# Performance work log

Measured on AMD Instinct MI355X. Metric: run time of the kernel, lower is better.

## Reference

```python
import jax, jax.numpy as jnp
import numpy as np

B, N, F_IN, F_OUT, H, SE_DIM = 16, 1024, 64, 64, 4, 64
ALPHA = 0.2  # LeakyReLU negative slope


def setup_inputs() -> dict:
    key = jax.random.key(0)
    ks = jax.random.split(key, 8)
    x = jax.random.normal(ks[0], (B, N, F_IN), dtype=jnp.float32)
    adj = (jax.random.uniform(ks[1], (B, N, N)) < 0.05).astype(jnp.float32)
    SE = jax.random.normal(ks[2], (N, SE_DIM), dtype=jnp.float32)
    fin = F_IN + SE_DIM
    s_w = float(np.sqrt(2.0) * np.sqrt(6.0 / (fin + F_OUT)))
    s_a = float(np.sqrt(2.0) * np.sqrt(6.0 / (F_OUT + 1)))
    s_p = float(np.sqrt(2.0) * np.sqrt(6.0 / (H + H)))
    W = jax.random.uniform(ks[3], (H, fin, F_OUT), minval=-s_w, maxval=s_w, dtype=jnp.float32)
    a1 = jax.random.uniform(ks[4], (H, F_OUT), minval=-s_a, maxval=s_a, dtype=jnp.float32)
    a2 = jax.random.uniform(ks[5], (H, F_OUT), minval=-s_a, maxval=s_a, dtype=jnp.float32)
    P_l = jax.random.uniform(ks[6], (H, H), minval=-s_p, maxval=s_p, dtype=jnp.float32)
    P_w = jax.random.uniform(ks[7], (H, H), minval=-s_p, maxval=s_p, dtype=jnp.float32)
    return {"x": x, "adj": adj, "SE": SE, "W": W, "a1": a1, "a2": a2, "P_l": P_l, "P_w": P_w}


def reference(x, adj, SE, W, a1, a2, P_l, P_w):
    b, n, _ = x.shape
    # needSE: concat positional/structural embedding (repeated over batch)
    xi = jnp.concatenate([x, jnp.broadcast_to(SE[None], (b, n, SE.shape[-1]))], axis=2)
    # per-head projection: h[b,h,n,o]
    h = jnp.einsum('bnf,hfo->bhno', xi, W)
    f1 = jnp.einsum('bhno,ho->bhn', h, a1)
    f2 = jnp.einsum('bhno,ho->bhn', h, a2)
    # e[b,h,i,j] = leaky_relu(f1[i] + f2[j])
    e = jax.nn.leaky_relu(f1[:, :, :, None] + f2[:, :, None, :], negative_slope=ALPHA)
    # talking-heads mixing before softmax (P_l); softmax over the i (row/source) axis
    e = jnp.einsum('bhij,hg->bgij', e, P_l)
    att = jax.nn.softmax(e, axis=2)
    # talking-heads mixing after softmax (P_w)
    att = jnp.einsum('bgij,gh->bhij', att, P_w)
    # adjacency masking (dropout p=0 -> identity)
    att = att * adj[:, None]
    # aggregation + residual (in == out features, no downsample) + ELU
    out = jnp.einsum('bhij,bhjo->bhio', att, h)
    out = jax.nn.elu(out + x[:, None])
    bb, hh, nn_, oo = out.shape
    # concat heads along feature dim (head order preserved)
    return out.transpose(0, 2, 1, 3).reshape(bb, nn_, hh * oo)
```

## Files before the change

### kernel.cpp

```cpp
#include <hip/hip_runtime.h>
#include <hip/hip_bf16.h>

#define NB 16
#define NN 1024
#define FOUT 64
#define NH 4
#define LRELU_A 0.2f
#define CAP 192

typedef __attribute__((ext_vector_type(8))) short bf16x8;
typedef __attribute__((ext_vector_type(4))) float f32x4;

#define WFENCE() asm volatile("s_waitcnt lgkmcnt(0)" ::: "memory")

__device__ __forceinline__ float lrelu(float s) { return fmaxf(s, LRELU_A * s); }

__device__ __forceinline__ float4 min4(float4 a, float4 b) {
    return make_float4(fminf(a.x,b.x), fminf(a.y,b.y), fminf(a.z,b.z), fminf(a.w,b.w));
}
__device__ __forceinline__ float4 max4(float4 a, float4 b) {
    return make_float4(fmaxf(a.x,b.x), fmaxf(a.y,b.y), fmaxf(a.z,b.z), fmaxf(a.w,b.w));
}

__device__ __forceinline__ unsigned int pk2(float a, float b) {
    union { __hip_bfloat16 h; unsigned short u; } ua, ub;
    ua.h = __float2bfloat16(a); ub.h = __float2bfloat16(b);
    return (unsigned int)ua.u | ((unsigned int)ub.u << 16);
}
__device__ __forceinline__ unsigned short bfbits(float a) {
    union { __hip_bfloat16 h; unsigned short u; } ua;
    ua.h = __float2bfloat16(a);
    return ua.u;
}
__device__ __forceinline__ int toff(int r, int c) { return (r * 16 + (c ^ (r & 7))) * 16; }

__global__ __launch_bounds__(256) void k_prep(const float* __restrict__ W,
                                              uint4* __restrict__ WbT)
{
    int gid  = blockIdx.x * 256 + threadIdx.x;
    int col  = gid >> 4, c = gid & 15;
    int head = col >> 6, o = col & 63;
    const float* wp = W + head * 8192 + (c * 8) * 64 + o;
    float v[8];
    #pragma unroll
    for (int j = 0; j < 8; ++j) v[j] = wp[j * 64];
    uint4 outv = { pk2(v[0], v[1]), pk2(v[2], v[3]), pk2(v[4], v[5]), pk2(v[6], v[7]) };
    WbT[col * 16 + (c ^ (col & 7))] = outv;
}

__global__ __launch_bounds__(256) void k_proj(const float* __restrict__ x,
                                              const float* __restrict__ SE,
                                              const uint4* __restrict__ WbT,
                                              unsigned int* __restrict__ hbu)
{
    __shared__ char smem[49152];
    char* Ab = smem;
    char* Bb = smem + 32768;
    const int tid = threadIdx.x;
    const int rt  = blockIdx.x >> 2;
    const int ch  = blockIdx.x & 3;

    {
        const int row = tid & 127, kh = tid >> 7;
        const int rg = rt * 128 + row;
        const int bb = rg >> 10, nn = rg & 1023;
        const float4* src = (kh == 0) ? (const float4*)(x + ((size_t)(bb * NN + nn)) * 64)
                                      : (const float4*)(SE + (size_t)nn * 64);
        #pragma unroll
        for (int q = 0; q < 8; ++q) {
            float4 u0 = src[q * 2], u1 = src[q * 2 + 1];
            uint4 pkv = { pk2(u0.x, u0.y), pk2(u0.z, u0.w), pk2(u1.x, u1.y), pk2(u1.z, u1.w) };
            *(uint4*)(Ab + toff(row, kh * 8 + q)) = pkv;
        }
    }
    {
        const uint4* wsrc = WbT + ch * 1024;
        #pragma unroll
        for (int q = 0; q < 4; ++q) ((uint4*)Bb)[tid + 256 * q] = wsrc[tid + 256 * q];
    }
    __syncthreads();

    const int l = tid & 63, w = tid >> 6;
    const int r0 = 32 * w + (l & 15);
    const int ci = l >> 4;
    f32x4 acc[2][4];
    #pragma unroll
    for (int a = 0; a < 2; ++a)
        #pragma unroll
        for (int bf = 0; bf < 4; ++bf) { acc[a][bf][0]=0.f; acc[a][bf][1]=0.f; acc[a][bf][2]=0.f; acc[a][bf][3]=0.f; }

    #pragma unroll
    for (int ks = 0; ks < 4; ++ks) {
        const int c = 4 * ks + ci;
        bf16x8 A0 = *(const bf16x8*)(Ab + toff(r0,      c));
        bf16x8 A1 = *(const bf16x8*)(Ab + toff(r0 + 16, c));
        #pragma unroll
        for (int bf = 0; bf < 4; ++bf) {
            bf16x8 Bf = *(const bf16x8*)(Bb + toff(16 * bf + (l & 15), c));
            acc[0][bf] = __builtin_amdgcn_mfma_f32_16x16x32_bf16(A0, Bf, acc[0][bf], 0, 0, 0);
            acc[1][bf] = __builtin_amdgcn_mfma_f32_16x16x32_bf16(A1, Bf, acc[1][bf], 0, 0, 0);
        }
    }
    __syncthreads();

    unsigned short* cst = (unsigned short*)smem + w * 2048;
    #pragma unroll
    for (int a = 0; a < 2; ++a)
        #pragma unroll
        for (int bf = 0; bf < 4; ++bf)
            #pragma unroll
            for (int reg = 0; reg < 4; ++reg) {
                int r   = 16 * a + (l >> 4) * 4 + reg;
                int col = 16 * bf + (l & 15);
                cst[r * 64 + col] = bfbits(acc[a][bf][reg]);
            }
    WFENCE();
    const uint4* csv = (const uint4*)cst;
    #pragma unroll
    for (int p = 0; p < 4; ++p) {
        int idx = p * 64 + l;
        uint4 v = csv[idx];
        int r = idx >> 3, o8 = idx & 7;
        int ng = rt * 128 + 32 * w + r;
        int bb = ng >> 10, n2 = ng & 1023;
        ((uint4*)hbu)[((size_t)(bb * NH + ch) * NN + n2) * 8 + o8] = v;
    }
}

__global__ __launch_bounds__(256) void k_f12(const unsigned short* __restrict__ hb,
                                             const float* __restrict__ a1,
                                             const float* __restrict__ a2,
                                             float* __restrict__ f1p,
                                             float* __restrict__ f2p)
{
    int task = blockIdx.x * 4 + (threadIdx.x >> 6);
    int lane = threadIdx.x & 63;
    int b = task >> 10, n = task & 1023;
    #pragma unroll
    for (int hh = 0; hh < NH; ++hh) {
        unsigned short us = hb[((size_t)(b * NH + hh) * NN + n) * 64 + lane];
        float v  = __uint_as_float((unsigned int)us << 16);
        float s1 = v * a1[hh * 64 + lane];
        float s2 = v * a2[hh * 64 + lane];
        #pragma unroll
        for (int m = 32; m > 0; m >>= 1) { s1 += __shfl_xor(s1, m); s2 += __shfl_xor(s2, m); }
        if (lane == 0) {
            f1p[(b * NN + n) * 4 + hh] = s1;
            f2p[(b * NN + n) * 4 + hh] = s2;
        }
    }
}

__global__ __launch_bounds__(256) void k_stats(const float* __restrict__ f1p,
                                               const float* __restrict__ f2p,
                                               const float* __restrict__ P_l,
                                               float* __restrict__ Mp,
                                               float* __restrict__ Rp)
{
    __shared__ float4 f1s[1024];
    __shared__ float4 red[8][32];
    const int tid  = threadIdx.x;
    const int lane = tid & 63;
    const int b   = blockIdx.x >> 5;
    const int jt  = blockIdx.x & 31;
    const float4* f1p4 = (const float4*)f1p;
    const float4* f2p4 = (const float4*)f2p;

    #pragma unroll
    for (int q = 0; q < 4; ++q) f1s[tid + 256 * q] = f1p4[b * NN + tid + 256 * q];
    __syncthreads();

    float4 mn = make_float4( INFINITY,  INFINITY,  INFINITY,  INFINITY);
    float4 mx = make_float4(-INFINITY, -INFINITY, -INFINITY, -INFINITY);
    #pragma unroll
    for (int q = 0; q < 16; ++q) {
        float4 v = f1s[lane + 64 * q];
        mn = min4(mn, v);
        mx = max4(mx, v);
    }
    #pragma unroll
    for (int m = 32; m > 0; m >>= 1) {
        float4 on = make_float4(__shfl_xor(mn.x, m), __shfl_xor(mn.y, m), __shfl_xor(mn.z, m), __shfl_xor(mn.w, m));
        float4 ox = make_float4(__shfl_xor(mx.x, m), __shfl_xor(mx.y, m), __shfl_xor(mx.z, m), __shfl_xor(mx.w, m));
        mn = min4(mn, on);
        mx = max4(mx, ox);
    }

    float pl[4][4];
    #pragma unroll
    for (int hh = 0; hh < 4; ++hh)
        #pragma unroll
        for (int g = 0; g < 4; ++g) pl[hh][g] = P_l[hh * 4 + g];

    const int jj = tid & 31, ic = tid >> 5;
    const int j  = jt * 32 + jj;
    float4 f2v = f2p4[b * NN + j];
    float f2a[4] = {f2v.x, f2v.y, f2v.z, f2v.w};
    float mna[4] = {mn.x, mn.y, mn.z, mn.w};
    float mxa[4] = {mx.x, mx.y, mx.z, mx.w};
    float mub[4];
    #pragma unroll
    for (int g = 0; g < 4; ++g) {
        float s = 0.f;
        #pragma unroll
        for (int hh = 0; hh < 4; ++hh) {
            float base = (pl[hh][g] >= 0.f ? mxa[hh] : mna[hh]) + f2a[hh];
            s = fmaf(pl[hh][g], lrelu(base), s);
        }
        mub[g] = s;
    }

    float d[4] = {0.f, 0.f, 0.f, 0.f};
    const int i0 = ic * 128;
    #pragma unroll 2
    for (int i = i0; i < i0 + 128; ++i) {
        float4 f1v = f1s[i];
        float l0 = lrelu(f1v.x + f2a[0]);
        float l1 = lrelu(f1v.y + f2a[1]);
        float l2 = lrelu(f1v.z + f2a[2]);
        float l3 = lrelu(f1v.w + f2a[3]);
        #pragma unroll
        for (int g = 0; g < 4; ++g) {
            float e = fmaf(pl[0][g], l0, fmaf(pl[1][g], l1, fmaf(pl[2][g], l2, pl[3][g] * l3)));
            d[g] += __expf(e - mub[g]);
        }
    }
    red[ic][jj] = make_float4(d[0], d[1], d[2], d[3]);
    __syncthreads();
    if (ic == 0) {
        float4 t = red[0][jj];
        #pragma unroll
        for (int r = 1; r < 8; ++r) {
            float4 u = red[r][jj];
            t.x += u.x; t.y += u.y; t.z += u.z; t.w += u.w;
        }
        ((float4*)Rp)[b * NN + j] = make_float4(1.f / t.x, 1.f / t.y, 1.f / t.z, 1.f / t.w);
        ((float4*)Mp)[b * NN + j] = make_float4(mub[0], mub[1], mub[2], mub[3]);
    }
}

__global__ __launch_bounds__(256) void k_agg(const float* __restrict__ adj,
                                             const float* __restrict__ x,
                                             const unsigned int* __restrict__ hb,
                                             const float* __restrict__ f1p,
                                             const float* __restrict__ f2p,
                                             const float* __restrict__ Mp,
                                             const float* __restrict__ Rp,
                                             const float* __restrict__ P_l,
                                             const float* __restrict__ P_w,
                                             float* __restrict__ out)
{
    __shared__ int   jl[4][CAP + 8];
    __shared__ float attlT[4][4][CAP + 8];
    const int tid  = threadIdx.x;
    const int w    = tid >> 6;
    const int lane = tid & 63;
    const int row  = blockIdx.x * 4 + w;
    const int b    = row >> 10;

    const float4* arow = (const float4*)adj + (size_t)row * 256;
    float4 av[4];
    #pragma unroll
    for (int q = 0; q < 4; ++q) av[q] = arow[lane + 64 * q];

    const unsigned long long lt = (1ull << lane) - 1ull;
    int cnt = 0;
    #pragma unroll
    for (int q = 0; q < 4; ++q) {
        float vv[4] = {av[q].x, av[q].y, av[q].z, av[q].w};
        #pragma unroll
        for (int c = 0; c < 4; ++c) {
            bool nz = (vv[c] != 0.f);
            unsigned long long mask = __ballot(nz);
            if (nz) {
                int pos = cnt + __popcll(mask & lt);
                if (pos < CAP) jl[w][pos] = (lane + 64 * q) * 4 + c;
            }
            cnt += __popcll(mask);
        }
    }
    if (cnt > CAP) cnt = CAP;
    WFENCE();

    float pl[4][4], pw[4][4];
    #pragma unroll
    for (int a_ = 0; a_ < 4; ++a_)
        #pragma unroll
        for (int g = 0; g < 4; ++g) {
            pl[a_][g] = P_l[a_ * 4 + g];
            pw[a_][g] = P_w[a_ * 4 + g];
        }
    const float4 f1v = ((const float4*)f1p)[row];
    for (int base = 0; base < cnt; base += 64) {
        int kk = base + lane;
        if (kk < cnt) {
            int j = jl[w][kk];
            float4 f2v = ((const float4*)f2p)[b * NN + j];
            float4 mv  = ((const float4*)Mp)[b * NN + j];
            float4 rv  = ((const float4*)Rp)[b * NN + j];
            float l0 = lrelu(f1v.x + f2v.x);
            float l1 = lrelu(f1v.y + f2v.y);
            float l2 = lrelu(f1v.z + f2v.z);
            float l3 = lrelu(f1v.w + f2v.w);
            float p0 = __expf(fmaf(pl[0][0], l0, fmaf(pl[1][0], l1, fmaf(pl[2][0], l2, pl[3][0] * l3))) - mv.x) * rv.x;
            float p1 = __expf(fmaf(pl[0][1], l0, fmaf(pl[1][1], l1, fmaf(pl[2][1], l2, pl[3][1] * l3))) - mv.y) * rv.y;
            float p2 = __expf(fmaf(pl[0][2], l0, fmaf(pl[1][2], l1, fmaf(pl[2][2], l2, pl[3][2] * l3))) - mv.z) * rv.z;
            float p3 = __expf(fmaf(pl[0][3], l0, fmaf(pl[1][3], l1, fmaf(pl[2][3], l2, pl[3][3] * l3))) - mv.w) * rv.w;
            #pragma unroll
            for (int g = 0; g < 4; ++g)
                attlT[w][g][kk] =
                    fmaf(p0, pw[0][g], fmaf(p1, pw[1][g], fmaf(p2, pw[2][g], p3 * pw[3][g])));
        }
    }
    if (lane < 8) {
        jl[w][cnt + lane] = 0;
        #pragma unroll
        for (int g = 0; g < 4; ++g) attlT[w][g][cnt + lane] = 0.f;
    }
    WFENCE();

    const int hh = lane >> 4;
    const int og = lane & 15;
    const uint2* hrow = (const uint2*)hb + ((size_t)(b * NH + hh) * NN) * 16 + og;
    const float* atp = &attlT[w][hh][0];
    float a0 = 0.f, a1_ = 0.f, a2_ = 0.f, a3_ = 0.f;
    #pragma unroll 1
    for (int base = 0; base < cnt; base += 8) {
        const int4   ja = *(const int4*)&jl[w][base];
        const int4   jb = *(const int4*)&jl[w][base + 4];
        const float4 ta = *(const float4*)&atp[base];
        const float4 tb = *(const float4*)&atp[base + 4];
        uint2 u0 = hrow[(size_t)ja.x * 16];
        uint2 u1 = hrow[(size_t)ja.y * 16];
        uint2 u2 = hrow[(size_t)ja.z * 16];
        uint2 u3 = hrow[(size_t)ja.w * 16];
        uint2 u4 = hrow[(size_t)jb.x * 16];
        uint2 u5 = hrow[(size_t)jb.y * 16];
        uint2 u6 = hrow[(size_t)jb.z * 16];
        uint2 u7 = hrow[(size_t)jb.w * 16];
        a0 = fmaf(ta.x, __uint_as_float(u0.x << 16), a0);
        a1_ = fmaf(ta.x, __uint_as_float(u0.x & 0xffff0000u), a1_);
        a2_ = fmaf(ta.x, __uint_as_float(u0.y << 16), a2_);
        a3_ = fmaf(ta.x, __uint_as_float(u0.y & 0xffff0000u), a3_);
        a0 = fmaf(ta.y, __uint_as_float(u1.x << 16), a0);
        a1_ = fmaf(ta.y, __uint_as_float(u1.x & 0xffff0000u), a1_);
        a2_ = fmaf(ta.y, __uint_as_float(u1.y << 16), a2_);
        a3_ = fmaf(ta.y, __uint_as_float(u1.y & 0xffff0000u), a3_);
        a0 = fmaf(ta.z, __uint_as_float(u2.x << 16), a0);
        a1_ = fmaf(ta.z, __uint_as_float(u2.x & 0xffff0000u), a1_);
        a2_ = fmaf(ta.z, __uint_as_float(u2.y << 16), a2_);
        a3_ = fmaf(ta.z, __uint_as_float(u2.y & 0xffff0000u), a3_);
        a0 = fmaf(ta.w, __uint_as_float(u3.x << 16), a0);
        a1_ = fmaf(ta.w, __uint_as_float(u3.x & 0xffff0000u), a1_);
        a2_ = fmaf(ta.w, __uint_as_float(u3.y << 16), a2_);
        a3_ = fmaf(ta.w, __uint_as_float(u3.y & 0xffff0000u), a3_);
        a0 = fmaf(tb.x, __uint_as_float(u4.x << 16), a0);
        a1_ = fmaf(tb.x, __uint_as_float(u4.x & 0xffff0000u), a1_);
        a2_ = fmaf(tb.x, __uint_as_float(u4.y << 16), a2_);
        a3_ = fmaf(tb.x, __uint_as_float(u4.y & 0xffff0000u), a3_);
        a0 = fmaf(tb.y, __uint_as_float(u5.x << 16), a0);
        a1_ = fmaf(tb.y, __uint_as_float(u5.x & 0xffff0000u), a1_);
        a2_ = fmaf(tb.y, __uint_as_float(u5.y << 16), a2_);
        a3_ = fmaf(tb.y, __uint_as_float(u5.y & 0xffff0000u), a3_);
        a0 = fmaf(tb.z, __uint_as_float(u6.x << 16), a0);
        a1_ = fmaf(tb.z, __uint_as_float(u6.x & 0xffff0000u), a1_);
        a2_ = fmaf(tb.z, __uint_as_float(u6.y << 16), a2_);
        a3_ = fmaf(tb.z, __uint_as_float(u6.y & 0xffff0000u), a3_);
        a0 = fmaf(tb.w, __uint_as_float(u7.x << 16), a0);
        a1_ = fmaf(tb.w, __uint_as_float(u7.x & 0xffff0000u), a1_);
        a2_ = fmaf(tb.w, __uint_as_float(u7.y << 16), a2_);
        a3_ = fmaf(tb.w, __uint_as_float(u7.y & 0xffff0000u), a3_);
    }
    float4 xr = ((const float4*)x)[row * 16 + og];
    float r0 = a0  + xr.x;
    float r1 = a1_ + xr.y;
    float r2 = a2_ + xr.z;
    float r3 = a3_ + xr.w;
    float4 o4;
    o4.x = (r0 > 0.f) ? r0 : (__expf(r0) - 1.f);
    o4.y = (r1 > 0.f) ? r1 : (__expf(r1) - 1.f);
    o4.z = (r2 > 0.f) ? r2 : (__expf(r2) - 1.f);
    o4.w = (r3 > 0.f) ? r3 : (__expf(r3) - 1.f);
    ((float4*)out)[(size_t)row * 64 + hh * 16 + og] = o4;
}

extern "C" void kernel_launch(void* const* d_in, const int* in_sizes, int n_in,
                              void* d_out, int out_size, void* d_ws, size_t ws_size,
                              hipStream_t stream)
{
    (void)in_sizes; (void)n_in; (void)out_size; (void)ws_size;
    const float* x   = (const float*)d_in[0];
    const float* adj = (const float*)d_in[1];
    const float* SE  = (const float*)d_in[2];
    const float* W   = (const float*)d_in[3];
    const float* a1  = (const float*)d_in[4];
    const float* a2  = (const float*)d_in[5];
    const float* P_l = (const float*)d_in[6];
    const float* P_w = (const float*)d_in[7];
    float* out = (float*)d_out;

    float* f1p = (float*)d_ws;
    float* f2p = f1p + 65536;
    float* Mp  = f2p + 65536;
    float* Rp  = Mp  + 65536;
    unsigned int* hbu = (unsigned int*)(Rp + 65536);
    uint4* WbT = (uint4*)(hbu + 2097152);

    k_prep <<<16,   256, 0, stream>>>(W, WbT);
    k_proj <<<512,  256, 0, stream>>>(x, SE, WbT, hbu);
    k_f12  <<<4096, 256, 0, stream>>>((const unsigned short*)hbu, a1, a2, f1p, f2p);
    k_stats<<<512,  256, 0, stream>>>(f1p, f2p, P_l, Mp, Rp);
    k_agg  <<<4096, 256, 0, stream>>>(adj, x, hbu, f1p, f2p, Mp, Rp, P_l, P_w, out);
}
```

Before: 189.6 us.

## Fuse weight prep and f1/f2 into projection; retile stats and aggregation gather

Drops k_prep by converting W to bf16 inside k_proj. Drops k_f12 by computing the f1/f2 attention logits from the MFMA accumulators with a 16-lane shuffle reduction, which removes a re-read of h and two launches. k_stats now launches four times as many blocks with a smaller j tile and a rotated i order. k_agg swizzles its block order and gathers 16-byte h rows, with the lane halves splitting the neighbour list and combining by shuffle. The tradeoffs are extra strided W loads in every projection block and more reduction work in k_stats.

```diff
diff --git a/kernel.cpp b/kernel.cpp
--- a/kernel.cpp
+++ b/kernel.cpp
@@ -34,24 +34,14 @@
 }
 __device__ __forceinline__ int toff(int r, int c) { return (r * 16 + (c ^ (r & 7))) * 16; }
 
-__global__ __launch_bounds__(256) void k_prep(const float* __restrict__ W,
-                                              uint4* __restrict__ WbT)
-{
-    int gid  = blockIdx.x * 256 + threadIdx.x;
-    int col  = gid >> 4, c = gid & 15;
-    int head = col >> 6, o = col & 63;
-    const float* wp = W + head * 8192 + (c * 8) * 64 + o;
-    float v[8];
-    #pragma unroll
-    for (int j = 0; j < 8; ++j) v[j] = wp[j * 64];
-    uint4 outv = { pk2(v[0], v[1]), pk2(v[2], v[3]), pk2(v[4], v[5]), pk2(v[6], v[7]) };
-    WbT[col * 16 + (c ^ (col & 7))] = outv;
-}
-
 __global__ __launch_bounds__(256) void k_proj(const float* __restrict__ x,
                                               const float* __restrict__ SE,
-                                              const uint4* __restrict__ WbT,
-                                              unsigned int* __restrict__ hbu)
+                                              const float* __restrict__ W,
+                                              const float* __restrict__ a1,
+                                              const float* __restrict__ a2,
+                                              unsigned int* __restrict__ hbu,
+                                              float* __restrict__ f1p,
+                                              float* __restrict__ f2p)
 {
     __shared__ char smem[49152];
     char* Ab = smem;
@@ -74,9 +64,18 @@
         }
     }
     {
-        const uint4* wsrc = WbT + ch * 1024;
-        #pragma unroll
-        for (int q = 0; q < 4; ++q) ((uint4*)Bb)[tid + 256 * q] = wsrc[tid + 256 * q];
+        const float* wbase = W + ch * 8192;
+        #pragma unroll
+        for (int q = 0; q < 4; ++q) {
+            int gid = tid + 256 * q;
+            int col = gid & 63, c = gid >> 6;
+            const float* wp = wbase + (c * 8) * 64 + col;
+            float v[8];
+            #pragma unroll
+            for (int j = 0; j < 8; ++j) v[j] = wp[j * 64];
+            uint4 pkv = { pk2(v[0], v[1]), pk2(v[2], v[3]), pk2(v[4], v[5]), pk2(v[6], v[7]) };
+            *(uint4*)(Bb + toff(col, c)) = pkv;
+        }
     }
     __syncthreads();
 
@@ -100,6 +99,38 @@
             acc[0][bf] = __builtin_amdgcn_mfma_f32_16x16x32_bf16(A0, Bf, acc[0][bf], 0, 0, 0);
             acc[1][bf] = __builtin_amdgcn_mfma_f32_16x16x32_bf16(A1, Bf, acc[1][bf], 0, 0, 0);
         }
+    }
+
+    {
+        float a1v[4], a2v[4];
+        #pragma unroll
+        for (int bf = 0; bf < 4; ++bf) {
+            a1v[bf] = a1[ch * 64 + 16 * bf + (l & 15)];
+            a2v[bf] = a2[ch * 64 + 16 * bf + (l & 15)];
+        }
+        #pragma unroll
+        for (int a = 0; a < 2; ++a)
+            #pragma unroll
+            for (int reg = 0; reg < 4; ++reg) {
+                float s1 = 0.f, s2 = 0.f;
+                #pragma unroll
+                for (int bf = 0; bf < 4; ++bf) {
+                    s1 = fmaf(acc[a][bf][reg], a1v[bf], s1);
+                    s2 = fmaf(acc[a][bf][reg], a2v[bf], s2);
+                }
+                #pragma unroll
+                for (int m = 1; m < 16; m <<= 1) {
+                    s1 += __shfl_xor(s1, m);
+                    s2 += __shfl_xor(s2, m);
+                }
+                if ((l & 15) == 0) {
+                    int r  = 16 * a + (l >> 4) * 4 + reg;
+                    int ng = rt * 128 + 32 * w + r;
+                    int bb = ng >> 10, n2 = ng & 1023;
+                    f1p[(bb * NN + n2) * 4 + ch] = s1;
+                    f2p[(bb * NN + n2) * 4 + ch] = s2;
+                }
+            }
     }
     __syncthreads();
 
@@ -127,30 +158,6 @@
     }
 }
 
-__global__ __launch_bounds__(256) void k_f12(const unsigned short* __restrict__ hb,
-                                             const float* __restrict__ a1,
-                                             const float* __restrict__ a2,
-                                             float* __restrict__ f1p,
-                                             float* __restrict__ f2p)
-{
-    int task = blockIdx.x * 4 + (threadIdx.x >> 6);
-    int lane = threadIdx.x & 63;
-    int b = task >> 10, n = task & 1023;
-    #pragma unroll
-    for (int hh = 0; hh < NH; ++hh) {
-        unsigned short us = hb[((size_t)(b * NH + hh) * NN + n) * 64 + lane];
-        float v  = __uint_as_float((unsigned int)us << 16);
-        float s1 = v * a1[hh * 64 + lane];
-        float s2 = v * a2[hh * 64 + lane];
-        #pragma unroll
-        for (int m = 32; m > 0; m >>= 1) { s1 += __shfl_xor(s1, m); s2 += __shfl_xor(s2, m); }
-        if (lane == 0) {
-            f1p[(b * NN + n) * 4 + hh] = s1;
-            f2p[(b * NN + n) * 4 + hh] = s2;
-        }
-    }
-}
-
 __global__ __launch_bounds__(256) void k_stats(const float* __restrict__ f1p,
                                                const float* __restrict__ f2p,
                                                const float* __restrict__ P_l,
@@ -158,11 +165,11 @@
                                                float* __restrict__ Rp)
 {
     __shared__ float4 f1s[1024];
-    __shared__ float4 red[8][32];
+    __shared__ float4 red[32][8];
     const int tid  = threadIdx.x;
     const int lane = tid & 63;
-    const int b   = blockIdx.x >> 5;
-    const int jt  = blockIdx.x & 31;
+    const int b    = blockIdx.x >> 7;
+    const int jt   = blockIdx.x & 127;
     const float4* f1p4 = (const float4*)f1p;
     const float4* f2p4 = (const float4*)f2p;
 
@@ -192,8 +199,8 @@
         #pragma unroll
         for (int g = 0; g < 4; ++g) pl[hh][g] = P_l[hh * 4 + g];
 
-    const int jj = tid & 31, ic = tid >> 5;
-    const int j  = jt * 32 + jj;
+    const int jj = tid & 7, ic = tid >> 3;
+    const int j  = jt * 8 + jj;
     float4 f2v = f2p4[b * NN + j];
     float f2a[4] = {f2v.x, f2v.y, f2v.z, f2v.w};
     float mna[4] = {mn.x, mn.y, mn.z, mn.w};
@@ -211,9 +218,9 @@
     }
 
     float d[4] = {0.f, 0.f, 0.f, 0.f};
-    const int i0 = ic * 128;
-    #pragma unroll 2
-    for (int i = i0; i < i0 + 128; ++i) {
+    #pragma unroll 4
+    for (int ii = 0; ii < 32; ++ii) {
+        int i = ic * 32 + ((ii + 2 * ic) & 31);
         float4 f1v = f1s[i];
         float l0 = lrelu(f1v.x + f2a[0]);
         float l1 = lrelu(f1v.y + f2a[1]);
@@ -227,11 +234,11 @@
     }
     red[ic][jj] = make_float4(d[0], d[1], d[2], d[3]);
     __syncthreads();
-    if (ic == 0) {
-        float4 t = red[0][jj];
-        #pragma unroll
-        for (int r = 1; r < 8; ++r) {
-            float4 u = red[r][jj];
+    if (tid < 8) {
+        float4 t = red[0][tid];
+        #pragma unroll
+        for (int r = 1; r < 32; ++r) {
+            float4 u = red[r][tid];
             t.x += u.x; t.y += u.y; t.z += u.z; t.w += u.w;
         }
         ((float4*)Rp)[b * NN + j] = make_float4(1.f / t.x, 1.f / t.y, 1.f / t.z, 1.f / t.w);
@@ -255,7 +262,9 @@
     const int tid  = threadIdx.x;
     const int w    = tid >> 6;
     const int lane = tid & 63;
-    const int row  = blockIdx.x * 4 + w;
+    const int orig = blockIdx.x;
+    const int swz  = (orig & 7) * 512 + (orig >> 3);
+    const int row  = swz * 4 + w;
     const int b    = row >> 10;
 
     const float4* arow = (const float4*)adj + (size_t)row * 256;
@@ -280,6 +289,7 @@
         }
     }
     if (cnt > CAP) cnt = CAP;
+    if (lane < 8) jl[w][cnt + lane] = 0;
     WFENCE();
 
     float pl[4][4], pw[4][4];
@@ -313,75 +323,91 @@
         }
     }
     if (lane < 8) {
-        jl[w][cnt + lane] = 0;
         #pragma unroll
         for (int g = 0; g < 4; ++g) attlT[w][g][cnt + lane] = 0.f;
     }
     WFENCE();
 
-    const int hh = lane >> 4;
-    const int og = lane & 15;
-    const uint2* hrow = (const uint2*)hb + ((size_t)(b * NH + hh) * NN) * 16 + og;
+    const int e2  = lane >> 5;
+    const int sub = lane & 31;
+    const int hh  = sub >> 3;
+    const int oct = sub & 7;
+    const uint4* hrow = (const uint4*)hb + ((size_t)(b * NH + hh) * NN) * 8 + oct;
     const float* atp = &attlT[w][hh][0];
-    float a0 = 0.f, a1_ = 0.f, a2_ = 0.f, a3_ = 0.f;
-    #pragma unroll 1
+    float acc[8];
+    #pragma unroll
+    for (int e = 0; e < 8; ++e) acc[e] = 0.f;
+
+    #pragma unroll 2
     for (int base = 0; base < cnt; base += 8) {
-        const int4   ja = *(const int4*)&jl[w][base];
-        const int4   jb = *(const int4*)&jl[w][base + 4];
-        const float4 ta = *(const float4*)&atp[base];
-        const float4 tb = *(const float4*)&atp[base + 4];
-        uint2 u0 = hrow[(size_t)ja.x * 16];
-        uint2 u1 = hrow[(size_t)ja.y * 16];
-        uint2 u2 = hrow[(size_t)ja.z * 16];
-        uint2 u3 = hrow[(size_t)ja.w * 16];
-        uint2 u4 = hrow[(size_t)jb.x * 16];
-        uint2 u5 = hrow[(size_t)jb.y * 16];
-        uint2 u6 = hrow[(size_t)jb.z * 16];
-        uint2 u7 = hrow[(size_t)jb.w * 16];
-        a0 = fmaf(ta.x, __uint_as_float(u0.x << 16), a0);
-        a1_ = fmaf(ta.x, __uint_as_float(u0.x & 0xffff0000u), a1_);
-        a2_ = fmaf(ta.x, __uint_as_float(u0.y << 16), a2_);
-        a3_ = fmaf(ta.x, __uint_as_float(u0.y & 0xffff0000u), a3_);
-        a0 = fmaf(ta.y, __uint_as_float(u1.x << 16), a0);
-        a1_ = fmaf(ta.y, __uint_as_float(u1.x & 0xffff0000u), a1_);
-        a2_ = fmaf(ta.y, __uint_as_float(u1.y << 16), a2_);
-        a3_ = fmaf(ta.y, __uint_as_float(u1.y & 0xffff0000u), a3_);
-        a0 = fmaf(ta.z, __uint_as_float(u2.x << 16), a0);
-        a1_ = fmaf(ta.z, __uint_as_float(u2.x & 0xffff0000u), a1_);
-        a2_ = fmaf(ta.z, __uint_as_float(u2.y << 16), a2_);
-        a3_ = fmaf(ta.z, __uint_as_float(u2.y & 0xffff0000u), a3_);
-        a0 = fmaf(ta.w, __uint_as_float(u3.x << 16), a0);
-        a1_ = fmaf(ta.w, __uint_as_float(u3.x & 0xffff0000u), a1_);
-        a2_ = fmaf(ta.w, __uint_as_float(u3.y << 16), a2_);
-        a3_ = fmaf(ta.w, __uint_as_float(u3.y & 0xffff0000u), a3_);
-        a0 = fmaf(tb.x, __uint_as_float(u4.x << 16), a0);
-        a1_ = fmaf(tb.x, __uint_as_float(u4.x & 0xffff0000u), a1_);
-        a2_ = fmaf(tb.x, __uint_as_float(u4.y << 16), a2_);
-        a3_ = fmaf(tb.x, __uint_as_float(u4.y & 0xffff0000u), a3_);
-        a0 = fmaf(tb.y, __uint_as_float(u5.x << 16), a0);
-        a1_ = fmaf(tb.y, __uint_as_float(u5.x & 0xffff0000u), a1_);
-        a2_ = fmaf(tb.y, __uint_as_float(u5.y << 16), a2_);
-        a3_ = fmaf(tb.y, __uint_as_float(u5.y & 0xffff0000u), a3_);
-        a0 = fmaf(tb.z, __uint_as_float(u6.x << 16), a0);
-        a1_ = fmaf(tb.z, __uint_as_float(u6.x & 0xffff0000u), a1_);
-        a2_ = fmaf(tb.z, __uint_as_float(u6.y << 16), a2_);
-        a3_ = fmaf(tb.z, __uint_as_float(u6.y & 0xffff0000u), a3_);
-        a0 = fmaf(tb.w, __uint_as_float(u7.x << 16), a0);
-        a1_ = fmaf(tb.w, __uint_as_float(u7.x & 0xffff0000u), a1_);
-        a2_ = fmaf(tb.w, __uint_as_float(u7.y << 16), a2_);
-        a3_ = fmaf(tb.w, __uint_as_float(u7.y & 0xffff0000u), a3_);
-    }
-    float4 xr = ((const float4*)x)[row * 16 + og];
-    float r0 = a0  + xr.x;
-    float r1 = a1_ + xr.y;
-    float r2 = a2_ + xr.z;
-    float r3 = a3_ + xr.w;
-    float4 o4;
-    o4.x = (r0 > 0.f) ? r0 : (__expf(r0) - 1.f);
-    o4.y = (r1 > 0.f) ? r1 : (__expf(r1) - 1.f);
-    o4.z = (r2 > 0.f) ? r2 : (__expf(r2) - 1.f);
-    o4.w = (r3 > 0.f) ? r3 : (__expf(r3) - 1.f);
-    ((float4*)out)[(size_t)row * 64 + hh * 16 + og] = o4;
+        int j0 = jl[w][base     + e2];
+        int j1 = jl[w][base + 2 + e2];
+        int j2 = jl[w][base + 4 + e2];
+        int j3 = jl[w][base + 6 + e2];
+        uint4 u0 = hrow[(size_t)j0 * 8];
+        uint4 u1 = hrow[(size_t)j1 * 8];
+        uint4 u2 = hrow[(size_t)j2 * 8];
+        uint4 u3 = hrow[(size_t)j3 * 8];
+        float t0 = atp[base     + e2];
+        float t1 = atp[base + 2 + e2];
+        float t2 = atp[base + 4 + e2];
+        float t3 = atp[base + 6 + e2];
+        acc[0] = fmaf(t0, __uint_as_float(u0.x << 16),          acc[0]);
+        acc[1] = fmaf(t0, __uint_as_float(u0.x & 0xffff0000u),  acc[1]);
+        acc[2] = fmaf(t0, __uint_as_float(u0.y << 16),          acc[2]);
+        acc[3] = fmaf(t0, __uint_as_float(u0.y & 0xffff0000u),  acc[3]);
+        acc[4] = fmaf(t0, __uint_as_float(u0.z << 16),          acc[4]);
+        acc[5] = fmaf(t0, __uint_as_float(u0.z & 0xffff0000u),  acc[5]);
+        acc[6] = fmaf(t0, __uint_as_float(u0.w << 16),          acc[6]);
+        acc[7] = fmaf(t0, __uint_as_float(u0.w & 0xffff0000u),  acc[7]);
+        acc[0] = fmaf(t1, __uint_as_float(u1.x << 16),          acc[0]);
+        acc[1] = fmaf(t1, __uint_as_float(u1.x & 0xffff0000u),  acc[1]);
+        acc[2] = fmaf(t1, __uint_as_float(u1.y << 16),          acc[2]);
+        acc[3] = fmaf(t1, __uint_as_float(u1.y & 0xffff0000u),  acc[3]);
+        acc[4] = fmaf(t1, __uint_as_float(u1.z << 16),          acc[4]);
+        acc[5] = fmaf(t1, __uint_as_float(u1.z & 0xffff0000u),  acc[5]);
+        acc[6] = fmaf(t1, __uint_as_float(u1.w << 16),          acc[6]);
+        acc[7] = fmaf(t1, __uint_as_float(u1.w & 0xffff0000u),  acc[7]);
+        acc[0] = fmaf(t2, __uint_as_float(u2.x << 16),          acc[0]);
+        acc[1] = fmaf(t2, __uint_as_float(u2.x & 0xffff0000u),  acc[1]);
+        acc[2] = fmaf(t2, __uint_as_float(u2.y << 16),          acc[2]);
+        acc[3] = fmaf(t2, __uint_as_float(u2.y & 0xffff0000u),  acc[3]);
+        acc[4] = fmaf(t2, __uint_as_float(u2.z << 16),          acc[4]);
+        acc[5] = fmaf(t2, __uint_as_float(u2.z & 0xffff0000u),  acc[5]);
+        acc[6] = fmaf(t2, __uint_as_float(u2.w << 16),          acc[6]);
+        acc[7] = fmaf(t2, __uint_as_float(u2.w & 0xffff0000u),  acc[7]);
+        acc[0] = fmaf(t3, __uint_as_float(u3.x << 16),          acc[0]);
+        acc[1] = fmaf(t3, __uint_as_float(u3.x & 0xffff0000u),  acc[1]);
+        acc[2] = fmaf(t3, __uint_as_float(u3.y << 16),          acc[2]);
+        acc[3] = fmaf(t3, __uint_as_float(u3.y & 0xffff0000u),  acc[3]);
+        acc[4] = fmaf(t3, __uint_as_float(u3.z << 16),          acc[4]);
+        acc[5] = fmaf(t3, __uint_as_float(u3.z & 0xffff0000u),  acc[5]);
+        acc[6] = fmaf(t3, __uint_as_float(u3.w << 16),          acc[6]);
+        acc[7] = fmaf(t3, __uint_as_float(u3.w & 0xffff0000u),  acc[7]);
+    }
+
+    #pragma unroll
+    for (int e = 0; e < 8; ++e) acc[e] += __shfl_xor(acc[e], 32);
+
+    if (e2 == 0) {
+        const float4* x4 = (const float4*)x;
+        float4 xa = x4[(size_t)row * 16 + oct * 2];
+        float4 xb = x4[(size_t)row * 16 + oct * 2 + 1];
+        float r0 = acc[0] + xa.x, r1 = acc[1] + xa.y, r2 = acc[2] + xa.z, r3 = acc[3] + xa.w;
+        float r4 = acc[4] + xb.x, r5 = acc[5] + xb.y, r6 = acc[6] + xb.z, r7 = acc[7] + xb.w;
+        float4 o4a, o4b;
+        o4a.x = (r0 > 0.f) ? r0 : (__expf(r0) - 1.f);
+        o4a.y = (r1 > 0.f) ? r1 : (__expf(r1) - 1.f);
+        o4a.z = (r2 > 0.f) ? r2 : (__expf(r2) - 1.f);
+        o4a.w = (r3 > 0.f) ? r3 : (__expf(r3) - 1.f);
+        o4b.x = (r4 > 0.f) ? r4 : (__expf(r4) - 1.f);
+        o4b.y = (r5 > 0.f) ? r5 : (__expf(r5) - 1.f);
+        o4b.z = (r6 > 0.f) ? r6 : (__expf(r6) - 1.f);
+        o4b.w = (r7 > 0.f) ? r7 : (__expf(r7) - 1.f);
+        float4* op = (float4*)out + (size_t)row * 64 + hh * 16 + oct * 2;
+        op[0] = o4a;
+        op[1] = o4b;
+    }
 }
 
 extern "C" void kernel_launch(void* const* d_in, const int* in_sizes, int n_in,
@@ -404,11 +430,8 @@
     float* Mp  = f2p + 65536;
     float* Rp  = Mp  + 65536;
     unsigned int* hbu = (unsigned int*)(Rp + 65536);
-    uint4* WbT = (uint4*)(hbu + 2097152);
-
-    k_prep <<<16,   256, 0, stream>>>(W, WbT);
-    k_proj <<<512,  256, 0, stream>>>(x, SE, WbT, hbu);
-    k_f12  <<<4096, 256, 0, stream>>>((const unsigned short*)hbu, a1, a2, f1p, f2p);
-    k_stats<<<512,  256, 0, stream>>>(f1p, f2p, P_l, Mp, Rp);
+
+    k_proj <<<512,  256, 0, stream>>>(x, SE, W, a1, a2, hbu, f1p, f2p);
+    k_stats<<<2048, 256, 0, stream>>>(f1p, f2p, P_l, Mp, Rp);
     k_agg  <<<4096, 256, 0, stream>>>(adj, x, hbu, f1p, f2p, Mp, Rp, P_l, P_w, out);
 }
```

Measured after the change: 171.9 us. -9.3%, faster.
